# Optimization experiments

Hardware: AMD Instinct MI355X
Metric: run time of the kernel (lower is better)

## Reference

```python
import jax, jax.numpy as jnp
import numpy as np

HEADS = 16
EMBED = 1024
HEAD_DIM = EMBED // HEADS


def setup_inputs() -> dict:
    k = jax.random.key(0)
    ks = jax.random.split(k, 8)
    N, L = 8, 1024
    s = 1.0 / np.sqrt(HEAD_DIM)
    return {
        "key": jax.random.normal(ks[0], (N, L, EMBED), jnp.float32),
        "query": jax.random.normal(ks[1], (N, L, EMBED), jnp.float32),
        "value": jax.random.normal(ks[2], (N, L, EMBED), jnp.float32),
        "mask": jnp.ones((N, 1, 1, L), jnp.int32),
        "Wq": jax.random.normal(ks[3], (HEAD_DIM, HEAD_DIM), jnp.float32) * s,
        "Wk": jax.random.normal(ks[4], (HEAD_DIM, HEAD_DIM), jnp.float32) * s,
        "Wv": jax.random.normal(ks[5], (HEAD_DIM, HEAD_DIM), jnp.float32) * s,
        "Wo": jax.random.normal(ks[6], (EMBED, EMBED), jnp.float32) * (1.0 / np.sqrt(EMBED)),
    }


def reference(key, query, value, mask, Wq, Wk, Wv, Wo):
    # NOTE: original torch code calls weights.masked_fill(...) without assignment,
    # which is a no-op, so `mask` is faithfully ignored here.
    N, Lq, E = query.shape
    Lk = key.shape[1]
    H, D = HEADS, E // HEADS
    q = query.reshape(N, Lq, H, D)
    k = key.reshape(N, Lk, H, D)
    v = value.reshape(N, Lk, H, D)
    # per-head linear with weight shared across heads: x @ W^T (torch Linear)
    q = jnp.einsum('nqhd,ed->nqhe', q, Wq)
    k = jnp.einsum('nkhd,ed->nkhe', k, Wk)
    v = jnp.einsum('nkhd,ed->nkhe', v, Wv)
    weights = jnp.einsum('nqhd,nkhd->nhqk', q, k)
    attn = jax.nn.softmax(weights / jnp.sqrt(jnp.asarray(E, weights.dtype)), axis=-1)
    out = jnp.einsum('nhqk,nkhd->nqhd', attn, v).reshape(N, Lq, E)
    return out @ Wo.T
```

## Files before the change

kernel.cpp:

```cpp
#include <hip/hip_runtime.h>
#include <hip/hip_bf16.h>

#define HEADS 16
#define HDIM  64
#define EMB   1024
#define NB    8
#define SEQ   1024

typedef __bf16 bf16_t;
typedef __bf16 bf16x8 __attribute__((ext_vector_type(8)));
typedef __bf16 bf16x4 __attribute__((ext_vector_type(4)));
typedef float  floatx4 __attribute__((ext_vector_type(4)));
typedef float  f32x16  __attribute__((ext_vector_type(16)));

union PkU { unsigned u; __bf16 h[2]; };
union W4U { unsigned u[4]; bf16x8 v; };

__device__ __forceinline__ bf16x8 load8bf(const bf16_t* p) { return *(const bf16x8*)p; }
__device__ __forceinline__ bf16x4 cvt4(float4 a) {
    bf16x4 r; r[0]=(bf16_t)a.x; r[1]=(bf16_t)a.y; r[2]=(bf16_t)a.z; r[3]=(bf16_t)a.w;
    return r;
}
__device__ __forceinline__ bf16x8 cvt8(float4 a, float4 b) {
    bf16x8 r;
    r[0]=(bf16_t)a.x; r[1]=(bf16_t)a.y; r[2]=(bf16_t)a.z; r[3]=(bf16_t)a.w;
    r[4]=(bf16_t)b.x; r[5]=(bf16_t)b.y; r[6]=(bf16_t)b.z; r[7]=(bf16_t)b.w;
    return r;
}

__global__ __launch_bounds__(256) void proj_kernel(
    const float* __restrict__ q_in, const float* __restrict__ k_in,
    const float* __restrict__ v_in,
    const float* __restrict__ Wq, const float* __restrict__ Wk,
    const float* __restrict__ Wv,
    bf16_t* __restrict__ qp, bf16_t* __restrict__ kp, bf16_t* __restrict__ vt)
{
    __shared__ __align__(16) bf16_t wl[64][72];
    __shared__ __align__(16) bf16_t lo[64][72];

    const int wave = threadIdx.x >> 6;
    const int lane = threadIdx.x & 63;
    const int m  = lane & 15;
    const int q4 = lane >> 4;
    const int op = blockIdx.y;

    const float* x = (op == 0) ? q_in : (op == 1) ? k_in : v_in;
    const float* W = (op == 0) ? Wq   : (op == 1) ? Wk   : Wv;

    {
        const int t  = threadIdx.x;
        const int f  = t >> 2;
        const int kg = (t & 3) * 16;
        #pragma unroll
        for (int j = 0; j < 4; ++j) {
            float4 v = *(const float4*)(W + f * 64 + kg + j * 4);
            *(bf16x4*)&wl[f][kg + j * 4] = cvt4(v);
        }
    }
    __syncthreads();

    if (op == 2) {
        const int nh = blockIdx.x >> 4;
        const int l0 = (blockIdx.x & 15) * 64;
        const int n  = nh >> 4;
        const int h  = nh & 15;

        const int la = l0 + wave * 16 + m;
        const float* xr = x + (size_t)(n * 16384 + la * 16 + h) * 64;
        float4 f0 = *(const float4*)(xr + q4 * 8);
        float4 f1 = *(const float4*)(xr + q4 * 8 + 4);
        float4 f2 = *(const float4*)(xr + 32 + q4 * 8);
        float4 f3 = *(const float4*)(xr + 32 + q4 * 8 + 4);
        bf16x8 a0 = cvt8(f0, f1);
        bf16x8 a1 = cvt8(f2, f3);

        floatx4 acc[4];
        #pragma unroll
        for (int sub = 0; sub < 4; ++sub) {
            bf16x8 b0 = load8bf(&wl[sub * 16 + m][q4 * 8]);
            bf16x8 b1 = load8bf(&wl[sub * 16 + m][32 + q4 * 8]);
            floatx4 z = {0.f, 0.f, 0.f, 0.f};
            z = __builtin_amdgcn_mfma_f32_16x16x32_bf16(a0, b0, z, 0, 0, 0);
            z = __builtin_amdgcn_mfma_f32_16x16x32_bf16(a1, b1, z, 0, 0, 0);
            acc[sub] = z;
        }

        #pragma unroll
        for (int sub = 0; sub < 4; ++sub) {
            #pragma unroll
            for (int r = 0; r < 4; r += 2) {
                PkU u; u.h[0] = (bf16_t)acc[sub][r]; u.h[1] = (bf16_t)acc[sub][r + 1];
                *(unsigned*)&lo[sub * 16 + m][wave * 16 + q4 * 4 + r] = u.u;
            }
        }
        __syncthreads();

        const int e  = threadIdx.x >> 2;
        const int lc = (threadIdx.x & 3) * 16;
        bf16_t* dst = vt + ((size_t)nh * 64 + e) * 1024 + l0 + lc;
        *(bf16x8*)dst       = *(const bf16x8*)&lo[e][lc];
        *(bf16x8*)(dst + 8) = *(const bf16x8*)&lo[e][lc + 8];
    } else {
        const int row0 = blockIdx.x * 64 + wave * 16;

        const float* xr = x + (size_t)(row0 + m) * 64;
        float4 f0 = *(const float4*)(xr + q4 * 8);
        float4 f1 = *(const float4*)(xr + q4 * 8 + 4);
        float4 f2 = *(const float4*)(xr + 32 + q4 * 8);
        float4 f3 = *(const float4*)(xr + 32 + q4 * 8 + 4);
        bf16x8 a0 = cvt8(f0, f1);
        bf16x8 a1 = cvt8(f2, f3);

        floatx4 acc[4];
        #pragma unroll
        for (int sub = 0; sub < 4; ++sub) {
            bf16x8 b0 = load8bf(&wl[sub * 16 + m][q4 * 8]);
            bf16x8 b1 = load8bf(&wl[sub * 16 + m][32 + q4 * 8]);
            floatx4 z = {0.f, 0.f, 0.f, 0.f};
            z = __builtin_amdgcn_mfma_f32_16x16x32_bf16(a0, b0, z, 0, 0, 0);
            z = __builtin_amdgcn_mfma_f32_16x16x32_bf16(a1, b1, z, 0, 0, 0);
            acc[sub] = z;
        }

        #pragma unroll
        for (int sub = 0; sub < 4; ++sub) {
            #pragma unroll
            for (int r = 0; r < 4; ++r) {
                lo[wave * 16 + q4 * 4 + r][sub * 16 + m] = (bf16_t)acc[sub][r];
            }
        }
        __syncthreads();

        const int gl = threadIdx.x >> 2;
        const int ec = (threadIdx.x & 3) * 16;
        const int g  = blockIdx.x * 64 + gl;
        const int n  = g >> 14;
        const int l  = (g >> 4) & 1023;
        const int h  = g & 15;
        const int nh = n * 16 + h;
        bf16_t* dst = ((op == 0) ? qp : kp) + ((size_t)nh * 1024 + l) * 64 + ec;
        *(bf16x8*)dst       = *(const bf16x8*)&lo[gl][ec];
        *(bf16x8*)(dst + 8) = *(const bf16x8*)&lo[gl][ec + 8];
    }
}

__global__ __launch_bounds__(256) void attn_kernel(
    bf16_t* __restrict__ qp, const bf16_t* __restrict__ kp,
    const bf16_t* __restrict__ vt)
{
    __shared__ __align__(16) bf16_t kl[2][64][64];
    __shared__ __align__(16) bf16_t vl[2][64][64];

    const int lane = threadIdx.x & 63;
    const int wave = threadIdx.x >> 6;
    const int q32  = lane & 31;
    const int hi   = lane >> 5;

    const int nh   = blockIdx.x & 127;
    const int qblk = blockIdx.x >> 7;

    bf16_t* Q = qp + (size_t)nh * 65536;
    const bf16_t* K = kp + (size_t)nh * 65536;
    const bf16_t* V = vt + (size_t)nh * 65536;

    const int qb = qblk * 128 + wave * 32;

    const int srow  = lane >> 3;
    const int sslot = lane & 7;
    const int ch    = sslot ^ srow;

    auto stage = [&](int b, int kb) {
        #pragma unroll
        for (int i = 0; i < 2; ++i) {
            const int rbase = wave * 16 + i * 8;
            const int row   = rbase + srow;
            __builtin_amdgcn_global_load_lds(
                (const __attribute__((address_space(1))) unsigned int*)(K + (size_t)(kb + row) * 64 + ch * 8),
                (__attribute__((address_space(3))) unsigned int*)(&kl[b][rbase][0]),
                16, 0, 0);
            __builtin_amdgcn_global_load_lds(
                (const __attribute__((address_space(1))) unsigned int*)(V + (size_t)row * 1024 + kb + ch * 8),
                (__attribute__((address_space(3))) unsigned int*)(&vl[b][rbase][0]),
                16, 0, 0);
        }
    };

    stage(0, 0);

    bf16x8 bq[4];
    #pragma unroll
    for (int sl = 0; sl < 4; ++sl)
        bq[sl] = load8bf(Q + (size_t)(qb + q32) * 64 + sl * 16 + hi * 8);

    f32x16 o0 = {0.f,0.f,0.f,0.f,0.f,0.f,0.f,0.f,0.f,0.f,0.f,0.f,0.f,0.f,0.f,0.f};
    f32x16 o1 = o0;
    float lsum = 0.f;
    const float CE = 1.4426950408889634f * 0.03125f;

    int cur = 0;
    __syncthreads();

    for (int kt = 0; kt < 16; ++kt) {
        if (kt < 15) stage(cur ^ 1, (kt + 1) * 64);

        #pragma unroll
        for (int kb32 = 0; kb32 < 2; ++kb32) {
            const int krow = kb32 * 32 + q32;
            f32x16 s = {0.f,0.f,0.f,0.f,0.f,0.f,0.f,0.f,0.f,0.f,0.f,0.f,0.f,0.f,0.f,0.f};
            __builtin_amdgcn_s_setprio(1);
            #pragma unroll
            for (int sl = 0; sl < 4; ++sl) {
                const int ck = ((sl * 2 + hi) ^ (krow & 7)) * 8;
                bf16x8 ka = load8bf(&kl[cur][krow][ck]);
                s = __builtin_amdgcn_mfma_f32_32x32x16_bf16(ka, bq[sl], s, 0, 0, 0);
            }
            __builtin_amdgcn_s_setprio(0);

            unsigned w[8];
            #pragma unroll
            for (int t = 0; t < 8; ++t) {
                float p0 = exp2f(s[2 * t]     * CE);
                float p1 = exp2f(s[2 * t + 1] * CE);
                lsum += p0 + p1;
                PkU u; u.h[0] = (bf16_t)p0; u.h[1] = (bf16_t)p1;
                w[t] = u.u;
            }

            bf16x8 va[4];
            #pragma unroll
            for (int db = 0; db < 2; ++db) {
                const int d = db * 32 + q32;
                #pragma unroll
                for (int c = 0; c < 2; ++c) {
                    const int cv = ((kb32 * 4 + c * 2 + hi) ^ (d & 7)) * 8;
                    va[db * 2 + c] = load8bf(&vl[cur][d][cv]);
                }
            }

            const unsigned e0 = (unsigned)__shfl_xor((int)(hi ? w[0] : w[2]), 32, 64);
            const unsigned e1 = (unsigned)__shfl_xor((int)(hi ? w[1] : w[3]), 32, 64);
            const unsigned e2 = (unsigned)__shfl_xor((int)(hi ? w[4] : w[6]), 32, 64);
            const unsigned e3 = (unsigned)__shfl_xor((int)(hi ? w[5] : w[7]), 32, 64);

            W4U b0v, b1v;
            b0v.u[0] = hi ? e0 : w[0];
            b0v.u[1] = hi ? e1 : w[1];
            b0v.u[2] = hi ? w[2] : e0;
            b0v.u[3] = hi ? w[3] : e1;
            b1v.u[0] = hi ? e2 : w[4];
            b1v.u[1] = hi ? e3 : w[5];
            b1v.u[2] = hi ? w[6] : e2;
            b1v.u[3] = hi ? w[7] : e3;

            __builtin_amdgcn_s_setprio(1);
            o0 = __builtin_amdgcn_mfma_f32_32x32x16_bf16(va[0], b0v.v, o0, 0, 0, 0);
            o0 = __builtin_amdgcn_mfma_f32_32x32x16_bf16(va[1], b1v.v, o0, 0, 0, 0);
            o1 = __builtin_amdgcn_mfma_f32_32x32x16_bf16(va[2], b0v.v, o1, 0, 0, 0);
            o1 = __builtin_amdgcn_mfma_f32_32x32x16_bf16(va[3], b1v.v, o1, 0, 0, 0);
            __builtin_amdgcn_s_setprio(0);
        }

        __syncthreads();
        cur ^= 1;
    }

    lsum += __shfl_xor(lsum, 32, 64);
    const float inv = 1.0f / lsum;

    #pragma unroll
    for (int g = 0; g < 4; ++g) {
        bf16x4 w0v, w1v;
        #pragma unroll
        for (int r = 0; r < 4; ++r) {
            w0v[r] = (bf16_t)(o0[g * 4 + r] * inv);
            w1v[r] = (bf16_t)(o1[g * 4 + r] * inv);
        }
        *(bf16x4*)(Q + (size_t)(qb + q32) * 64 +      g * 8 + hi * 4) = w0v;
        *(bf16x4*)(Q + (size_t)(qb + q32) * 64 + 32 + g * 8 + hi * 4) = w1v;
    }
}

__global__ __launch_bounds__(256) void wocvt_kernel(
    const float* __restrict__ Wo, bf16_t* __restrict__ wo_bf)
{
    const int i = (blockIdx.x * 256 + threadIdx.x) * 8;
    float4 f0 = *(const float4*)(Wo + i);
    float4 f1 = *(const float4*)(Wo + i + 4);
    *(bf16x8*)(wo_bf + i) = cvt8(f0, f1);
}

__global__ __launch_bounds__(256) void outproj_kernel(
    const bf16_t* __restrict__ aoq, const bf16_t* __restrict__ wo_bf,
    float* __restrict__ out)
{
    __shared__ __align__(16) bf16_t wl[128][72];

    const int wave = threadIdx.x >> 6;
    const int lane = threadIdx.x & 63;
    const int m  = lane & 15;
    const int q4 = lane >> 4;

    const int bx = blockIdx.x >> 3;
    const int by = blockIdx.x & 7;

    const int row0 = bx * 128 + wave * 32;
    const int col0 = by * 128;

    const int ts_f = threadIdx.x >> 1;
    const int ts_k = (threadIdx.x & 1) * 32;

    floatx4 acc[2][8];
    #pragma unroll
    for (int rs = 0; rs < 2; ++rs)
        #pragma unroll
        for (int cs = 0; cs < 8; ++cs) acc[rs][cs] = (floatx4){0.f, 0.f, 0.f, 0.f};

    for (int h = 0; h < 16; ++h) {
        const int kc = h * 64;
        __syncthreads();
        #pragma unroll
        for (int j = 0; j < 4; ++j) {
            *(bf16x8*)&wl[ts_f][ts_k + j * 8] =
                load8bf(wo_bf + (size_t)(col0 + ts_f) * 1024 + kc + ts_k + j * 8);
        }
        __syncthreads();

        bf16x8 a[2][2];
        #pragma unroll
        for (int rs = 0; rs < 2; ++rs) {
            const int g = row0 + rs * 16 + m;
            const int n = g >> 10;
            const int q = g & 1023;
            const bf16_t* arow = aoq + ((size_t)(n * 16 + h) * 1024 + q) * 64;
            a[rs][0] = load8bf(arow + q4 * 8);
            a[rs][1] = load8bf(arow + 32 + q4 * 8);
        }

        #pragma unroll
        for (int cs = 0; cs < 8; ++cs) {
            bf16x8 b0 = load8bf(&wl[cs * 16 + m][q4 * 8]);
            bf16x8 b1 = load8bf(&wl[cs * 16 + m][32 + q4 * 8]);
            #pragma unroll
            for (int rs = 0; rs < 2; ++rs) {
                acc[rs][cs] = __builtin_amdgcn_mfma_f32_16x16x32_bf16(a[rs][0], b0, acc[rs][cs], 0, 0, 0);
                acc[rs][cs] = __builtin_amdgcn_mfma_f32_16x16x32_bf16(a[rs][1], b1, acc[rs][cs], 0, 0, 0);
            }
        }
    }

    #pragma unroll
    for (int rs = 0; rs < 2; ++rs) {
        #pragma unroll
        for (int r = 0; r < 4; ++r) {
            const int g = row0 + rs * 16 + q4 * 4 + r;
            #pragma unroll
            for (int cs = 0; cs < 8; ++cs)
                out[(size_t)g * 1024 + col0 + cs * 16 + m] = acc[rs][cs][r];
        }
    }
}

extern "C" void kernel_launch(void* const* d_in, const int* in_sizes, int n_in,
                              void* d_out, int out_size, void* d_ws, size_t ws_size,
                              hipStream_t stream) {
    const float* key   = (const float*)d_in[0];
    const float* query = (const float*)d_in[1];
    const float* value = (const float*)d_in[2];
    const float* Wq = (const float*)d_in[4];
    const float* Wk = (const float*)d_in[5];
    const float* Wv = (const float*)d_in[6];
    const float* Wo = (const float*)d_in[7];

    const size_t TENS = (size_t)NB * SEQ * EMB;
    bf16_t* qp = (bf16_t*)d_ws;
    bf16_t* vt = qp + TENS;
    bf16_t* kp = (bf16_t*)d_out;

    hipLaunchKernelGGL(proj_kernel, dim3(2048, 3), dim3(256), 0, stream,
                       query, key, value, Wq, Wk, Wv, qp, kp, vt);
    hipLaunchKernelGGL(attn_kernel, dim3(1024), dim3(256), 0, stream, qp, kp, vt);
    hipLaunchKernelGGL(wocvt_kernel, dim3(512), dim3(256), 0, stream, Wo, vt);
    hipLaunchKernelGGL(outproj_kernel, dim3(512), dim3(256), 0, stream,
                       qp, vt, (float*)d_out);
}
```

Before: 264.8 us.

## Fuse Wo conversion into output projection with double-buffered prefetch and smaller row tiles

Drops the separate fp32-to-bf16 Wo conversion kernel and converts Wo on the fly inside the output projection. Weight tiles for the next head are prefetched into registers and written into a double-buffered shared tile, so each iteration needs one barrier instead of two. Row tile per block is halved so twice as many blocks launch. In exchange each block reads fp32 weights and the weight matrix is re-read by more blocks, raising L2 traffic and reducing operand reuse per wave.

```diff
diff --git a/kernel.cpp b/kernel.cpp
--- a/kernel.cpp
+++ b/kernel.cpp
@@ -280,20 +280,11 @@
     }
 }
 
-__global__ __launch_bounds__(256) void wocvt_kernel(
-    const float* __restrict__ Wo, bf16_t* __restrict__ wo_bf)
-{
-    const int i = (blockIdx.x * 256 + threadIdx.x) * 8;
-    float4 f0 = *(const float4*)(Wo + i);
-    float4 f1 = *(const float4*)(Wo + i + 4);
-    *(bf16x8*)(wo_bf + i) = cvt8(f0, f1);
-}
-
 __global__ __launch_bounds__(256) void outproj_kernel(
-    const bf16_t* __restrict__ aoq, const bf16_t* __restrict__ wo_bf,
+    const bf16_t* __restrict__ aoq, const float* __restrict__ Wo,
     float* __restrict__ out)
 {
-    __shared__ __align__(16) bf16_t wl[128][72];
+    __shared__ __align__(16) bf16_t wl[2][128][72];
 
     const int wave = threadIdx.x >> 6;
     const int lane = threadIdx.x & 63;
@@ -303,60 +294,61 @@
     const int bx = blockIdx.x >> 3;
     const int by = blockIdx.x & 7;
 
-    const int row0 = bx * 128 + wave * 32;
+    const int row0 = bx * 64 + wave * 16;
     const int col0 = by * 128;
+
+    const int g_a = row0 + m;
+    const int n_a = g_a >> 10;
+    const int q_a = g_a & 1023;
 
     const int ts_f = threadIdx.x >> 1;
     const int ts_k = (threadIdx.x & 1) * 32;
 
-    floatx4 acc[2][8];
-    #pragma unroll
-    for (int rs = 0; rs < 2; ++rs)
-        #pragma unroll
-        for (int cs = 0; cs < 8; ++cs) acc[rs][cs] = (floatx4){0.f, 0.f, 0.f, 0.f};
-
+    const float* wsrc = Wo + (size_t)(col0 + ts_f) * 1024 + ts_k;
+
+    floatx4 acc[8];
+    #pragma unroll
+    for (int cs = 0; cs < 8; ++cs) acc[cs] = (floatx4){0.f, 0.f, 0.f, 0.f};
+
+    float4 wv[8];
+    #pragma unroll
+    for (int j = 0; j < 8; ++j) wv[j] = *(const float4*)(wsrc + j * 4);
+
+    int cur = 0;
     for (int h = 0; h < 16; ++h) {
-        const int kc = h * 64;
+        #pragma unroll
+        for (int p = 0; p < 4; ++p)
+            *(bf16x8*)&wl[cur][ts_f][ts_k + p * 8] = cvt8(wv[2 * p], wv[2 * p + 1]);
+
+        if (h < 15) {
+            const float* ws = wsrc + (h + 1) * 64;
+            #pragma unroll
+            for (int j = 0; j < 8; ++j) wv[j] = *(const float4*)(ws + j * 4);
+        }
+
         __syncthreads();
-        #pragma unroll
-        for (int j = 0; j < 4; ++j) {
-            *(bf16x8*)&wl[ts_f][ts_k + j * 8] =
-                load8bf(wo_bf + (size_t)(col0 + ts_f) * 1024 + kc + ts_k + j * 8);
-        }
-        __syncthreads();
-
-        bf16x8 a[2][2];
-        #pragma unroll
-        for (int rs = 0; rs < 2; ++rs) {
-            const int g = row0 + rs * 16 + m;
-            const int n = g >> 10;
-            const int q = g & 1023;
-            const bf16_t* arow = aoq + ((size_t)(n * 16 + h) * 1024 + q) * 64;
-            a[rs][0] = load8bf(arow + q4 * 8);
-            a[rs][1] = load8bf(arow + 32 + q4 * 8);
-        }
+
+        const bf16_t* arow = aoq + ((size_t)(n_a * 16 + h) * 1024 + q_a) * 64;
+        bf16x8 a0 = load8bf(arow + q4 * 8);
+        bf16x8 a1 = load8bf(arow + 32 + q4 * 8);
 
         #pragma unroll
         for (int cs = 0; cs < 8; ++cs) {
-            bf16x8 b0 = load8bf(&wl[cs * 16 + m][q4 * 8]);
-            bf16x8 b1 = load8bf(&wl[cs * 16 + m][32 + q4 * 8]);
-            #pragma unroll
-            for (int rs = 0; rs < 2; ++rs) {
-                acc[rs][cs] = __builtin_amdgcn_mfma_f32_16x16x32_bf16(a[rs][0], b0, acc[rs][cs], 0, 0, 0);
-                acc[rs][cs] = __builtin_amdgcn_mfma_f32_16x16x32_bf16(a[rs][1], b1, acc[rs][cs], 0, 0, 0);
-            }
-        }
-    }
-
-    #pragma unroll
-    for (int rs = 0; rs < 2; ++rs) {
-        #pragma unroll
-        for (int r = 0; r < 4; ++r) {
-            const int g = row0 + rs * 16 + q4 * 4 + r;
-            #pragma unroll
-            for (int cs = 0; cs < 8; ++cs)
-                out[(size_t)g * 1024 + col0 + cs * 16 + m] = acc[rs][cs][r];
-        }
+            bf16x8 b0 = load8bf(&wl[cur][cs * 16 + m][q4 * 8]);
+            bf16x8 b1 = load8bf(&wl[cur][cs * 16 + m][32 + q4 * 8]);
+            acc[cs] = __builtin_amdgcn_mfma_f32_16x16x32_bf16(a0, b0, acc[cs], 0, 0, 0);
+            acc[cs] = __builtin_amdgcn_mfma_f32_16x16x32_bf16(a1, b1, acc[cs], 0, 0, 0);
+        }
+
+        cur ^= 1;
+    }
+
+    #pragma unroll
+    for (int r = 0; r < 4; ++r) {
+        const int g = row0 + q4 * 4 + r;
+        #pragma unroll
+        for (int cs = 0; cs < 8; ++cs)
+            out[(size_t)g * 1024 + col0 + cs * 16 + m] = acc[cs][r];
     }
 }
 
@@ -379,7 +371,6 @@
     hipLaunchKernelGGL(proj_kernel, dim3(2048, 3), dim3(256), 0, stream,
                        query, key, value, Wq, Wk, Wv, qp, kp, vt);
     hipLaunchKernelGGL(attn_kernel, dim3(1024), dim3(256), 0, stream, qp, kp, vt);
-    hipLaunchKernelGGL(wocvt_kernel, dim3(512), dim3(256), 0, stream, Wo, vt);
-    hipLaunchKernelGGL(outproj_kernel, dim3(512), dim3(256), 0, stream,
-                       qp, vt, (float*)d_out);
-}
+    hipLaunchKernelGGL(outproj_kernel, dim3(1024), dim3(256), 0, stream,
+                       qp, Wo, (float*)d_out);
+}
```

Result: slower. 300.3 us (+13.4%).
